# Performance work log

Hardware: AMD Instinct MI355X
Metric: run time of the kernel (lower is better)

The kernel has to match this reference:

```python
import jax, jax.numpy as jnp
import numpy as np

T, HQ, HKV, D, R = 2048, 16, 4, 128, 8
NEG = -1e30


def apply_rope(x, cos, sin):
    # x: [T, H, D]; cos/sin: [T, D//2]; non-interleaved rotary over full head dim
    c = jnp.concatenate([cos, cos], axis=-1)[:, None, :]  # [T,1,D]
    s = jnp.concatenate([sin, sin], axis=-1)[:, None, :]
    half = x.shape[-1] // 2
    x1, x2 = x[..., :half], x[..., half:]
    rot = jnp.concatenate([-x2, x1], axis=-1)
    return x * c + rot * s


def setup_inputs() -> dict:
    key = jax.random.key(0)
    kq, kk, kv = jax.random.split(key, 3)
    q = jax.random.normal(kq, (T, HQ, D), dtype=jnp.float32)
    k = jax.random.normal(kk, (T, HKV, D), dtype=jnp.float32)
    v = jax.random.normal(kv, (T, HKV, D), dtype=jnp.float32)
    # standard rotary tables
    inv_freq = 1.0 / (10000.0 ** (np.arange(0, D, 2, dtype=np.float32) / D))
    ang = np.arange(T, dtype=np.float32)[:, None] * inv_freq[None, :]  # [T, D/2]
    cos = jnp.asarray(np.cos(ang), dtype=jnp.float32)
    sin = jnp.asarray(np.sin(ang), dtype=jnp.float32)
    # block-causal ranges: q block r attends to keys [0, (r+1)*B)
    B = T // R
    q_ranges = jnp.asarray([[r * B, (r + 1) * B] for r in range(R)], dtype=jnp.int32)
    k_ranges = jnp.asarray([[0, (r + 1) * B] for r in range(R)], dtype=jnp.int32)
    return {"q": q, "k": k, "v": v, "cos": cos, "sin": sin,
            "q_ranges": q_ranges, "k_ranges": k_ranges}


def reference(q, k, v, cos, sin, q_ranges, k_ranges):
    scale = 1.0 / jnp.sqrt(jnp.float32(D))
    qh = apply_rope(q, cos, sin)
    kh = apply_rope(k, cos, sin)
    rep = HQ // HKV
    kr = jnp.repeat(kh, rep, axis=1)  # [T,HQ,D]
    vr = jnp.repeat(v, rep, axis=1)
    idx = jnp.arange(T)
    qm = (idx[None, :] >= q_ranges[:, :1]) & (idx[None, :] < q_ranges[:, 1:])  # [R,T]
    km = (idx[None, :] >= k_ranges[:, :1]) & (idx[None, :] < k_ranges[:, 1:])  # [R,T]
    mask = jnp.any(qm[:, :, None] & km[:, None, :], axis=0)  # [T,T] union over ranges
    scores = jnp.einsum('qhd,khd->hqk', qh, kr) * scale  # [HQ,T,T]
    scores = jnp.where(mask[None], scores, NEG)
    p = jax.nn.softmax(scores, axis=-1)
    row_valid = jnp.any(mask, axis=-1)  # [T]
    p = jnp.where(row_valid[None, :, None], p, 0.0)  # uncovered q rows output zero
    out = jnp.einsum('hqk,khd->qhd', p, vr)
    return out
```

## Files before the change

### kernel.cpp

```cpp
#include <hip/hip_runtime.h>
#include <hip/hip_bf16.h>

#define T_   2048
#define HQ_  16
#define HKV_ 4
#define D_   128
#define QBLK 64
#define NQB  (T_/QBLK)
#define KVBLK 64

typedef float f32x4 __attribute__((ext_vector_type(4)));
typedef float f32x8 __attribute__((ext_vector_type(8)));
typedef __bf16 bf16x8 __attribute__((ext_vector_type(8)));
typedef unsigned short u16;
typedef unsigned short u16x8 __attribute__((ext_vector_type(8)));
typedef unsigned long long u64;

__device__ __forceinline__ u16 f2bf(float f) {
  unsigned u = __builtin_bit_cast(unsigned, f);
  u += 0x7FFFu + ((u >> 16) & 1u);
  return (u16)(u >> 16);
}

__global__ __launch_bounds__(256) void prep_qk(
    const float* __restrict__ q, const float* __restrict__ k,
    const float* __restrict__ ct, const float* __restrict__ st,
    u16* __restrict__ qr, u16* __restrict__ kr)
{
  const float scale = 0.08838834764831845f;
  const int NQT = T_ * HQ_ * 8;
  int gid = blockIdx.x * 256 + threadIdx.x;
  if (gid < NQT) {
    int j0 = (gid & 7) * 8;
    int h  = (gid >> 3) & 15;
    int t  = gid >> 7;
    const float* base = q + ((size_t)t * HQ_ + h) * D_;
    const float* cb = ct + t * 64 + j0;
    const float* sb = st + t * 64 + j0;
    u16 lo[8], hi[8];
#pragma unroll
    for (int e = 0; e < 8; ++e) {
      float x1 = base[j0 + e], x2 = base[j0 + 64 + e];
      float c = cb[e], s = sb[e];
      lo[e] = f2bf((x1 * c - x2 * s) * scale);
      hi[e] = f2bf((x2 * c + x1 * s) * scale);
    }
    u16* orow = qr + ((size_t)h * T_ + t) * D_;
    *reinterpret_cast<u16x8*>(orow + j0)      = *reinterpret_cast<u16x8*>(lo);
    *reinterpret_cast<u16x8*>(orow + 64 + j0) = *reinterpret_cast<u16x8*>(hi);
  } else {
    int th = gid - NQT;
    int j0 = (th & 7) * 8;
    int hh = (th >> 3) & 3;
    int t  = th >> 5;
    const float* base = k + ((size_t)t * HKV_ + hh) * D_;
    const float* cb = ct + t * 64 + j0;
    const float* sb = st + t * 64 + j0;
    u16 lo[8], hi[8];
#pragma unroll
    for (int e = 0; e < 8; ++e) {
      float x1 = base[j0 + e], x2 = base[j0 + 64 + e];
      float c = cb[e], s = sb[e];
      lo[e] = f2bf(x1 * c - x2 * s);
      hi[e] = f2bf(x2 * c + x1 * s);
    }
    u16* orow = kr + ((size_t)hh * T_ + t) * D_;
    *reinterpret_cast<u16x8*>(orow + j0)      = *reinterpret_cast<u16x8*>(lo);
    *reinterpret_cast<u16x8*>(orow + 64 + j0) = *reinterpret_cast<u16x8*>(hi);
  }
}

__global__ __launch_bounds__(256) void prep_v(
    const float* __restrict__ v, u16* __restrict__ vt)
{
  __shared__ __attribute__((aligned(16))) char L[128 * 144];
  const int tid = threadIdx.x;
  const int hh  = blockIdx.x & 3;
  const int t0  = (blockIdx.x >> 2) * 64;

  {
    int r  = tid >> 2;
    int d0 = (tid & 3) * 32;
    const float* row = v + ((size_t)(t0 + r) * HKV_ + hh) * D_ + d0;
#pragma unroll
    for (int e = 0; e < 32; ++e) {
      *reinterpret_cast<u16*>(L + (size_t)(d0 + e) * 144 + r * 2) = f2bf(row[e]);
    }
  }
  __syncthreads();
  {
    int d = tid >> 1;
    int half = tid & 1;
    u16* orow = vt + ((size_t)hh * D_ + d) * T_ + t0 + half * 32;
    const char* src = L + (size_t)d * 144 + half * 64;
#pragma unroll
    for (int j = 0; j < 4; ++j)
      *reinterpret_cast<u16x8*>(orow + j * 8) =
          *reinterpret_cast<const u16x8*>(src + j * 16);
  }
}

__global__ __launch_bounds__(256, 3) void attn_fwd(
    const u16* __restrict__ qr, const u16* __restrict__ kr,
    const u16* __restrict__ vt, float* __restrict__ out)
{
  __shared__ __attribute__((aligned(16))) char lds[16384 + 16384 + 8192];
  char* Klds  = lds;
  char* VTlds = lds + 16384;

  const int tid  = threadIdx.x;
  const int lane = tid & 63;
  const int wv   = tid >> 6;
  char* Plds = lds + 32768 + wv * 2048;

  const int bid = blockIdx.x;
  const int qb  = (NQB - 1) - (bid >> 4);
  const int h   = bid & 15;
  const int hkv = h >> 2;
  const int q0  = qb * QBLK + wv * 16;
  const int nt  = ((qb >> 2) + 1) * 4;

  const int lm = lane & 15;
  const int lh = lane >> 4;

  bf16x8 qf[4];
  {
    const u16* qrow = qr + ((size_t)h * T_ + q0 + lm) * D_;
#pragma unroll
    for (int kb = 0; kb < 4; ++kb)
      qf[kb] = *reinterpret_cast<const bf16x8*>(qrow + kb * 32 + lh * 8);
  }

  const u16* kbase = kr + (size_t)hkv * T_ * D_;
  const u16* vbase = vt + (size_t)hkv * D_ * T_;

  bf16x8 kpf[4], vpf[4];
#pragma unroll
  for (int j = 0; j < 4; ++j) {
    kpf[j] = *reinterpret_cast<const bf16x8*>(kbase + j * 2048 + tid * 8);
    int d = j * 32 + (tid >> 3);
    vpf[j] = *reinterpret_cast<const bf16x8*>(vbase + (size_t)d * T_ + (tid & 7) * 8);
  }

  f32x4 accO[8];
#pragma unroll
  for (int c = 0; c < 8; ++c) accO[c] = (f32x4){0.f, 0.f, 0.f, 0.f};
  float mrun = -1e30f, lrun = 0.f;

  for (int t = 0; t < nt; ++t) {
    __syncthreads();
#pragma unroll
    for (int j = 0; j < 4; ++j) {
      int off = j * 4096 + tid * 16;
      int row = off >> 8;
      *reinterpret_cast<bf16x8*>(Klds + (off ^ ((row & 7) << 4))) = kpf[j];
      int d = j * 32 + (tid >> 3);
      int offv = d * 128 + (tid & 7) * 16;
      *reinterpret_cast<bf16x8*>(VTlds + (offv ^ ((d & 7) << 4))) = vpf[j];
    }
    if (t + 1 < nt) {
      const u16* kb2 = kbase + (size_t)(t + 1) * KVBLK * D_;
      const u16* vb2 = vbase + (size_t)(t + 1) * KVBLK;
#pragma unroll
      for (int j = 0; j < 4; ++j) {
        kpf[j] = *reinterpret_cast<const bf16x8*>(kb2 + j * 2048 + tid * 8);
        int d = j * 32 + (tid >> 3);
        vpf[j] = *reinterpret_cast<const bf16x8*>(vb2 + (size_t)d * T_ + (tid & 7) * 8);
      }
    }
    __syncthreads();

    f32x4 s[4];
#pragma unroll
    for (int g = 0; g < 4; ++g) s[g] = (f32x4){0.f, 0.f, 0.f, 0.f};
    __builtin_amdgcn_s_setprio(1);
#pragma unroll
    for (int kb = 0; kb < 4; ++kb) {
#pragma unroll
      for (int g = 0; g < 4; ++g) {
        int row = lm + 16 * g;
        bf16x8 kf = *reinterpret_cast<const bf16x8*>(
            Klds + ((row * 256 + kb * 64 + lh * 16) ^ ((row & 7) << 4)));
        s[g] = __builtin_amdgcn_mfma_f32_16x16x32_bf16(kf, qf[kb], s[g], 0, 0, 0);
      }
    }
    __builtin_amdgcn_s_setprio(0);

    float tmax = -1e30f;
#pragma unroll
    for (int g = 0; g < 4; ++g)
      tmax = fmaxf(tmax, fmaxf(fmaxf(s[g][0], s[g][1]), fmaxf(s[g][2], s[g][3])));
    tmax = fmaxf(tmax, __shfl_xor(tmax, 16));
    tmax = fmaxf(tmax, __shfl_xor(tmax, 32));
    float mnew  = fmaxf(mrun, tmax);
    float alpha = __expf(mrun - mnew);
    float psum = 0.f;
#pragma unroll
    for (int g = 0; g < 4; ++g) {
      float p0 = __expf(s[g][0] - mnew), p1 = __expf(s[g][1] - mnew);
      float p2 = __expf(s[g][2] - mnew), p3 = __expf(s[g][3] - mnew);
      psum += (p0 + p1) + (p2 + p3);
      u64 w = (u64)f2bf(p0) | ((u64)f2bf(p1) << 16) |
              ((u64)f2bf(p2) << 32) | ((u64)f2bf(p3) << 48);
      *reinterpret_cast<u64*>(
          Plds + lm * 128 + ((g * 32 + lh * 8) ^ ((lm & 7) << 4))) = w;
    }
    psum += __shfl_xor(psum, 16);
    psum += __shfl_xor(psum, 32);
    lrun = lrun * alpha + psum;
    mrun = mnew;
#pragma unroll
    for (int c = 0; c < 8; ++c) {
      accO[c][0] *= alpha; accO[c][1] *= alpha;
      accO[c][2] *= alpha; accO[c][3] *= alpha;
    }

    bf16x8 pf[2];
#pragma unroll
    for (int half = 0; half < 2; ++half)
      pf[half] = *reinterpret_cast<const bf16x8*>(
          Plds + lm * 128 + ((half * 64 + lh * 16) ^ ((lm & 7) << 4)));
    __builtin_amdgcn_s_setprio(1);
#pragma unroll
    for (int c = 0; c < 8; ++c) {
#pragma unroll
      for (int half = 0; half < 2; ++half) {
        int row = c * 16 + lm;
        bf16x8 vf = *reinterpret_cast<const bf16x8*>(
            VTlds + ((row * 128 + half * 64 + lh * 16) ^ ((row & 7) << 4)));
        accO[c] = __builtin_amdgcn_mfma_f32_16x16x32_bf16(vf, pf[half], accO[c], 0, 0, 0);
      }
    }
    __builtin_amdgcn_s_setprio(0);
  }

  float inv = 1.f / lrun;
  float* orow = out + ((size_t)(q0 + lm) * HQ_ + h) * D_ + lh * 4;
#pragma unroll
  for (int c = 0; c < 8; ++c) {
    f32x4 o;
    o[0] = accO[c][0] * inv; o[1] = accO[c][1] * inv;
    o[2] = accO[c][2] * inv; o[3] = accO[c][3] * inv;
    *reinterpret_cast<f32x4*>(orow + c * 16) = o;
  }
}

extern "C" void kernel_launch(void* const* d_in, const int* in_sizes, int n_in,
                              void* d_out, int out_size, void* d_ws, size_t ws_size,
                              hipStream_t stream) {
  const float* q  = (const float*)d_in[0];
  const float* k  = (const float*)d_in[1];
  const float* v  = (const float*)d_in[2];
  const float* ct = (const float*)d_in[3];
  const float* st = (const float*)d_in[4];

  u16* qr = (u16*)d_ws;
  u16* kr = qr + (size_t)T_ * HQ_ * D_;
  u16* vt = kr + (size_t)T_ * HKV_ * D_;
  float* out = (float*)d_out;

  const int NQT = T_ * HQ_ * 8, NKT = T_ * HKV_ * 8;
  prep_qk<<<(NQT + NKT) / 256, 256, 0, stream>>>(q, k, ct, st, qr, kr);
  prep_v<<<HKV_ * (T_ / 64), 256, 0, stream>>>(v, vt);
  attn_fwd<<<NQB * HQ_, 256, 0, stream>>>(qr, kr, vt, out);
}
```

Before: 137.2 us.

## Merge prep kernels and double-buffer K/V LDS tiles to drop a barrier

```diff
diff --git a/kernel.cpp b/kernel.cpp
--- a/kernel.cpp
+++ b/kernel.cpp
@@ -10,7 +10,6 @@
 #define KVBLK 64
 
 typedef float f32x4 __attribute__((ext_vector_type(4)));
-typedef float f32x8 __attribute__((ext_vector_type(8)));
 typedef __bf16 bf16x8 __attribute__((ext_vector_type(8)));
 typedef unsigned short u16;
 typedef unsigned short u16x8 __attribute__((ext_vector_type(8)));
@@ -22,96 +21,95 @@
   return (u16)(u >> 16);
 }
 
-__global__ __launch_bounds__(256) void prep_qk(
+#define QK_BLOCKS 1280
+__global__ __launch_bounds__(256) void prep_all(
     const float* __restrict__ q, const float* __restrict__ k,
-    const float* __restrict__ ct, const float* __restrict__ st,
-    u16* __restrict__ qr, u16* __restrict__ kr)
+    const float* __restrict__ v, const float* __restrict__ ct,
+    const float* __restrict__ st,
+    u16* __restrict__ qr, u16* __restrict__ kr, u16* __restrict__ vt)
 {
-  const float scale = 0.08838834764831845f;
-  const int NQT = T_ * HQ_ * 8;
-  int gid = blockIdx.x * 256 + threadIdx.x;
-  if (gid < NQT) {
-    int j0 = (gid & 7) * 8;
-    int h  = (gid >> 3) & 15;
-    int t  = gid >> 7;
-    const float* base = q + ((size_t)t * HQ_ + h) * D_;
-    const float* cb = ct + t * 64 + j0;
-    const float* sb = st + t * 64 + j0;
-    u16 lo[8], hi[8];
-#pragma unroll
-    for (int e = 0; e < 8; ++e) {
-      float x1 = base[j0 + e], x2 = base[j0 + 64 + e];
-      float c = cb[e], s = sb[e];
-      lo[e] = f2bf((x1 * c - x2 * s) * scale);
-      hi[e] = f2bf((x2 * c + x1 * s) * scale);
-    }
-    u16* orow = qr + ((size_t)h * T_ + t) * D_;
-    *reinterpret_cast<u16x8*>(orow + j0)      = *reinterpret_cast<u16x8*>(lo);
-    *reinterpret_cast<u16x8*>(orow + 64 + j0) = *reinterpret_cast<u16x8*>(hi);
+  __shared__ __attribute__((aligned(16))) char Lv[32 * 144];
+  const int tid = threadIdx.x;
+  const int bid = blockIdx.x;
+  if (bid < QK_BLOCKS) {
+    const float scale = 0.08838834764831845f;
+    const int NQT = T_ * HQ_ * 8;
+    int gid = bid * 256 + tid;
+    if (gid < NQT) {
+      int j0 = (gid & 7) * 8;
+      int h  = (gid >> 3) & 15;
+      int t  = gid >> 7;
+      const float* base = q + ((size_t)t * HQ_ + h) * D_;
+      const float* cb = ct + t * 64 + j0;
+      const float* sb = st + t * 64 + j0;
+      u16 lo[8], hi[8];
+#pragma unroll
+      for (int e = 0; e < 8; ++e) {
+        float x1 = base[j0 + e], x2 = base[j0 + 64 + e];
+        float c = cb[e], s = sb[e];
+        lo[e] = f2bf((x1 * c - x2 * s) * scale);
+        hi[e] = f2bf((x2 * c + x1 * s) * scale);
+      }
+      u16* orow = qr + ((size_t)h * T_ + t) * D_;
+      *reinterpret_cast<u16x8*>(orow + j0)      = *reinterpret_cast<u16x8*>(lo);
+      *reinterpret_cast<u16x8*>(orow + 64 + j0) = *reinterpret_cast<u16x8*>(hi);
+    } else {
+      int th = gid - NQT;
+      int j0 = (th & 7) * 8;
+      int hh = (th >> 3) & 3;
+      int t  = th >> 5;
+      const float* base = k + ((size_t)t * HKV_ + hh) * D_;
+      const float* cb = ct + t * 64 + j0;
+      const float* sb = st + t * 64 + j0;
+      u16 lo[8], hi[8];
+#pragma unroll
+      for (int e = 0; e < 8; ++e) {
+        float x1 = base[j0 + e], x2 = base[j0 + 64 + e];
+        float c = cb[e], s = sb[e];
+        lo[e] = f2bf(x1 * c - x2 * s);
+        hi[e] = f2bf(x2 * c + x1 * s);
+      }
+      u16* orow = kr + ((size_t)hh * T_ + t) * D_;
+      *reinterpret_cast<u16x8*>(orow + j0)      = *reinterpret_cast<u16x8*>(lo);
+      *reinterpret_cast<u16x8*>(orow + 64 + j0) = *reinterpret_cast<u16x8*>(hi);
+    }
   } else {
-    int th = gid - NQT;
-    int j0 = (th & 7) * 8;
-    int hh = (th >> 3) & 3;
-    int t  = th >> 5;
-    const float* base = k + ((size_t)t * HKV_ + hh) * D_;
-    const float* cb = ct + t * 64 + j0;
-    const float* sb = st + t * 64 + j0;
-    u16 lo[8], hi[8];
-#pragma unroll
-    for (int e = 0; e < 8; ++e) {
-      float x1 = base[j0 + e], x2 = base[j0 + 64 + e];
-      float c = cb[e], s = sb[e];
-      lo[e] = f2bf(x1 * c - x2 * s);
-      hi[e] = f2bf(x2 * c + x1 * s);
-    }
-    u16* orow = kr + ((size_t)hh * T_ + t) * D_;
-    *reinterpret_cast<u16x8*>(orow + j0)      = *reinterpret_cast<u16x8*>(lo);
-    *reinterpret_cast<u16x8*>(orow + 64 + j0) = *reinterpret_cast<u16x8*>(hi);
-  }
-}
-
-__global__ __launch_bounds__(256) void prep_v(
-    const float* __restrict__ v, u16* __restrict__ vt)
-{
-  __shared__ __attribute__((aligned(16))) char L[128 * 144];
-  const int tid = threadIdx.x;
-  const int hh  = blockIdx.x & 3;
-  const int t0  = (blockIdx.x >> 2) * 64;
-
-  {
-    int r  = tid >> 2;
-    int d0 = (tid & 3) * 32;
-    const float* row = v + ((size_t)(t0 + r) * HKV_ + hh) * D_ + d0;
-#pragma unroll
-    for (int e = 0; e < 32; ++e) {
-      *reinterpret_cast<u16*>(L + (size_t)(d0 + e) * 144 + r * 2) = f2bf(row[e]);
-    }
-  }
-  __syncthreads();
-  {
-    int d = tid >> 1;
-    int half = tid & 1;
-    u16* orow = vt + ((size_t)hh * D_ + d) * T_ + t0 + half * 32;
-    const char* src = L + (size_t)d * 144 + half * 64;
-#pragma unroll
-    for (int j = 0; j < 4; ++j)
-      *reinterpret_cast<u16x8*>(orow + j * 8) =
-          *reinterpret_cast<const u16x8*>(src + j * 16);
-  }
-}
-
-__global__ __launch_bounds__(256, 3) void attn_fwd(
+    int vbid = bid - QK_BLOCKS;
+    int hh = vbid & 3;
+    int t0 = ((vbid >> 2) & 31) * 64;
+    int d0 = (vbid >> 7) * 32;
+    {
+      int r  = tid >> 2;
+      int dg = tid & 3;
+      const float* vrow = v + ((size_t)(t0 + r) * HKV_ + hh) * D_ + d0 + dg * 8;
+      float4 f0 = *reinterpret_cast<const float4*>(vrow);
+      float4 f1 = *reinterpret_cast<const float4*>(vrow + 4);
+      float fv[8] = {f0.x, f0.y, f0.z, f0.w, f1.x, f1.y, f1.z, f1.w};
+#pragma unroll
+      for (int e = 0; e < 8; ++e)
+        *reinterpret_cast<u16*>(Lv + (dg * 8 + e) * 144 + r * 2) = f2bf(fv[e]);
+    }
+    __syncthreads();
+    {
+      int dl = tid >> 3;
+      int c0 = (tid & 7) * 16;
+      u16x8 val = *reinterpret_cast<const u16x8*>(Lv + dl * 144 + c0);
+      u16* orow = vt + ((size_t)(hh * D_ + d0 + dl)) * T_ + t0 + (c0 >> 1);
+      *reinterpret_cast<u16x8*>(orow) = val;
+    }
+  }
+}
+
+__global__ __launch_bounds__(256, 2) void attn_fwd(
     const u16* __restrict__ qr, const u16* __restrict__ kr,
     const u16* __restrict__ vt, float* __restrict__ out)
 {
-  __shared__ __attribute__((aligned(16))) char lds[16384 + 16384 + 8192];
-  char* Klds  = lds;
-  char* VTlds = lds + 16384;
+  __shared__ __attribute__((aligned(16))) char lds[73728];
 
   const int tid  = threadIdx.x;
   const int lane = tid & 63;
   const int wv   = tid >> 6;
-  char* Plds = lds + 32768 + wv * 2048;
+  char* Plds = lds + 65536 + wv * 2048;
 
   const int bid = blockIdx.x;
   const int qb  = (NQB - 1) - (bid >> 4);
@@ -148,7 +146,8 @@
   float mrun = -1e30f, lrun = 0.f;
 
   for (int t = 0; t < nt; ++t) {
-    __syncthreads();
+    char* Klds  = lds + (t & 1) * 16384;
+    char* VTlds = lds + 32768 + (t & 1) * 16384;
 #pragma unroll
     for (int j = 0; j < 4; ++j) {
       int off = j * 4096 + tid * 16;
@@ -259,8 +258,6 @@
   u16* vt = kr + (size_t)T_ * HKV_ * D_;
   float* out = (float*)d_out;
 
-  const int NQT = T_ * HQ_ * 8, NKT = T_ * HKV_ * 8;
-  prep_qk<<<(NQT + NKT) / 256, 256, 0, stream>>>(q, k, ct, st, qr, kr);
-  prep_v<<<HKV_ * (T_ / 64), 256, 0, stream>>>(v, vt);
+  prep_all<<<QK_BLOCKS + 512, 256, 0, stream>>>(q, k, v, ct, st, qr, kr, vt);
   attn_fwd<<<NQB * HQ_, 256, 0, stream>>>(qr, kr, vt, out);
 }
```

Result: faster. 133.0 us (-3.1%).
